# Optimization experiments

Measured on AMD Instinct MI355X. Metric: run time of the kernel, lower is better.

The kernel has to match this reference:

```python
import jax, jax.numpy as jnp
import numpy as np

B, L, D, H = 2, 2048, 1024, 16


def setup_inputs() -> dict:
    key = jax.random.key(0)
    ks = jax.random.split(key, 6)
    return {
        "x": jax.random.normal(ks[0], (B, L, D), dtype=jnp.float32),
        "w_qkv": jax.random.normal(ks[1], (3 * D, D), dtype=jnp.float32) * (D ** -0.5),
        "b_qkv": jax.random.normal(ks[2], (3 * D,), dtype=jnp.float32) * 0.02,
        "w_out": jax.random.normal(ks[3], (D, D), dtype=jnp.float32) * (D ** -0.5),
        "b_out": jax.random.normal(ks[4], (D,), dtype=jnp.float32) * 0.02,
        "lam": jnp.float32(0.5),
        "heads": H,
    }


def reference(x, w_qkv, b_qkv, w_out, b_out, lam, heads):
    b, l, d = x.shape
    dh = d // heads
    scale = d ** -0.5  # NOTE: module scales by d_model**-0.5, not head_dim**-0.5

    qkv = x @ w_qkv.T + b_qkv                      # [B, L, 3D]
    qkv = qkv.reshape(b, l, 3, heads, dh)
    qkv = jnp.transpose(qkv, (2, 0, 3, 1, 4))      # [3, B, H, L, dh]
    q, k, v = qkv[0], qkv[1], qkv[2]

    k_prev = jnp.roll(k, shift=1, axis=2)          # roll along sequence dim

    s_cur = jnp.einsum("bhqd,bhkd->bhqk", q, k) * scale
    s_prev = jnp.einsum("bhqd,bhkd->bhqk", q, k_prev) * scale

    a1 = jax.nn.softmax(s_cur, axis=-1)
    a2 = jax.nn.softmax(s_prev, axis=-1)
    diff = lam * (a1 - a2)                         # dropout = identity (eval)

    o = jnp.einsum("bhqk,bhkd->bhqd", diff, v)     # [B, H, L, dh]
    o = jnp.transpose(o, (0, 2, 1, 3)).reshape(b, l, d)
    return o @ w_out.T + b_out
```

## Files before the change

### kernel.cpp

```cpp
#include <hip/hip_runtime.h>
#include <hip/hip_bf16.h>
#include <stdint.h>


typedef __attribute__((ext_vector_type(8))) short s16x8;
typedef __attribute__((ext_vector_type(4))) short s16x4;
typedef __attribute__((ext_vector_type(4))) float f32x4;
typedef __attribute__((ext_vector_type(4))) unsigned int u32x4;

__device__ __forceinline__ float bf2f(unsigned short u) {
    union { unsigned int i; float f; } x; x.i = ((unsigned int)u) << 16; return x.f;
}
__device__ __forceinline__ unsigned short f2bf(float f) {
    union { float f; unsigned int i; } x; x.f = f;
    unsigned int r = x.i + 0x7FFFu + ((x.i >> 16) & 1u);
    return (unsigned short)(r >> 16);
}

__device__ __forceinline__ void gload16(const void* g, void* l) {
    auto gp = reinterpret_cast<const __attribute__((address_space(1))) unsigned int*>(
        reinterpret_cast<uintptr_t>(g));
    auto lp = reinterpret_cast<__attribute__((address_space(3))) unsigned int*>(
        reinterpret_cast<uintptr_t>(l));
    __builtin_amdgcn_global_load_lds(gp, lp, 16, 0, 0);
}

__global__ __launch_bounds__(256) void cvt_all(
    const float* __restrict__ x, const float* __restrict__ wq,
    const float* __restrict__ wo,
    unsigned short* __restrict__ xb, unsigned short* __restrict__ wqb,
    unsigned short* __restrict__ wob)
{
    int i4 = blockIdx.x * 256 + threadIdx.x;
    const float* src; unsigned short* dst; int off;
    if (i4 < 1048576)            { src = x;  dst = xb;  off = i4; }
    else if (i4 < 1048576 + 786432) { src = wq; dst = wqb; off = i4 - 1048576; }
    else                         { src = wo; dst = wob; off = i4 - 1835008; }
    float4 v = ((const float4*)src)[off];
    ushort4 u;
    u.x = f2bf(v.x); u.y = f2bf(v.y); u.z = f2bf(v.z); u.w = f2bf(v.w);
    ((ushort4*)dst)[off] = u;
}

__global__ __launch_bounds__(256) void vd_transpose(
    const unsigned short* __restrict__ qkvb, unsigned short* __restrict__ vdt)
{
    __shared__ unsigned short T[64][72];
    const int tid = threadIdx.x;
    const int j0 = blockIdx.x * 64;
    const int bh = blockIdx.y, b = bh >> 4, h = bh & 15;
    const unsigned short* vb = qkvb + (size_t)b * 2048 * 3072 + 2048 + h * 64;

    int r = tid >> 2, cq = tid & 3;
    int rp = (r & 35) | ((r & 12) << 1) | ((r & 16) >> 2);
    int j = j0 + r, jn = (j + 1) & 2047;
    const unsigned short* p0 = vb + (size_t)j  * 3072 + cq * 16;
    const unsigned short* p1 = vb + (size_t)jn * 3072 + cq * 16;
    s16x8 a0 = *(const s16x8*)p0, a1 = *(const s16x8*)(p0 + 8);
    s16x8 b0 = *(const s16x8*)p1, b1 = *(const s16x8*)(p1 + 8);
#pragma unroll
    for (int u = 0; u < 8; ++u)
        T[cq * 16 + u][rp] = f2bf(bf2f((unsigned short)a0[u]) - bf2f((unsigned short)b0[u]));
#pragma unroll
    for (int u = 0; u < 8; ++u)
        T[cq * 16 + 8 + u][rp] = f2bf(bf2f((unsigned short)a1[u]) - bf2f((unsigned short)b1[u]));
    __syncthreads();

    int row = tid >> 2, sc = tid & 3;
    s16x8 o0 = *(const s16x8*)&T[row][sc * 16];
    s16x8 o1 = *(const s16x8*)&T[row][sc * 16 + 8];
    unsigned short* dst = vdt + ((size_t)bh * 64 + row) * 2048 + j0 + sc * 16;
    *(s16x8*)dst = o0;
    *(s16x8*)(dst + 8) = o1;
}

template <int OUT_BF16, int BN>
__global__ __launch_bounds__(256) void gemm_nt_mfma(
    const unsigned short* __restrict__ A,
    const unsigned short* __restrict__ Bm,
    const float* __restrict__ bias,
    void* __restrict__ C,
    int M, int N, int K, int nscale, float smul)
{
    constexpr int NT = BN / 32;
    __shared__ unsigned short As[2][128][32];
    __shared__ unsigned short Bs[2][BN][32];

    const int tid = threadIdx.x;
    const int wave = tid >> 6, lane = tid & 63;
    const int quad = lane >> 4, ln = lane & 15;
    const int wm = (wave >> 1) * 64, wn = (wave & 1) * (NT * 16);
    const int m0 = blockIdx.y * 128, n0 = blockIdx.x * BN;
    const int rA = wave * 16 + (lane >> 2);
    const int gsl = lane & 3;

    f32x4 acc[4][NT];
#pragma unroll
    for (int mt = 0; mt < 4; ++mt)
#pragma unroll
        for (int nt = 0; nt < NT; ++nt) acc[mt][nt] = f32x4{0.f, 0.f, 0.f, 0.f};

    auto stage = [&](int p, int k0) {
#pragma unroll
        for (int q = 0; q < 2; ++q) {
            int row = q * 64 + rA;
            int kg = gsl ^ ((row >> 1) & 3);
            gload16(A + (size_t)(m0 + row) * K + k0 + kg * 8,
                    &As[p][q * 64 + wave * 16][0]);
            if (q * 64 < BN)
                gload16(Bm + (size_t)(n0 + row) * K + k0 + kg * 8,
                        &Bs[p][q * 64 + wave * 16][0]);
        }
    };

    stage(0, 0);
    __syncthreads();
    int p = 0;
    for (int k0 = 0; k0 < K; k0 += 32) {
        if (k0 + 32 < K) stage(p ^ 1, k0 + 32);
        s16x8 af[4], bfr[NT];
#pragma unroll
        for (int mt = 0; mt < 4; ++mt) {
            int rr = wm + mt * 16 + ln;
            af[mt] = *(const s16x8*)&As[p][rr][((quad ^ ((rr >> 1) & 3)) & 3) * 8];
        }
#pragma unroll
        for (int nt = 0; nt < NT; ++nt) {
            int rr = wn + nt * 16 + ln;
            bfr[nt] = *(const s16x8*)&Bs[p][rr][((quad ^ ((rr >> 1) & 3)) & 3) * 8];
        }
#pragma unroll
        for (int mt = 0; mt < 4; ++mt)
#pragma unroll
            for (int nt = 0; nt < NT; ++nt)
                acc[mt][nt] = __builtin_amdgcn_mfma_f32_16x16x32_bf16(
                    af[mt], bfr[nt], acc[mt][nt], 0, 0, 0);
        __syncthreads();
        p ^= 1;
    }

    float bb[NT];
#pragma unroll
    for (int nt = 0; nt < NT; ++nt) bb[nt] = bias[n0 + wn + nt * 16 + ln];
#pragma unroll
    for (int mt = 0; mt < 4; ++mt)
#pragma unroll
        for (int nt = 0; nt < NT; ++nt) {
            int col = n0 + wn + nt * 16 + ln;
            float sc = (col < nscale) ? smul : 1.f;
#pragma unroll
            for (int rg = 0; rg < 4; ++rg) {
                int row = m0 + wm + mt * 16 + quad * 4 + rg;
                float v = (acc[mt][nt][rg] + bb[nt]) * sc;
                if (OUT_BF16)
                    ((unsigned short*)C)[(size_t)row * N + col] = f2bf(v);
                else
                    ((float*)C)[(size_t)row * N + col] = v;
            }
        }
}

__global__ __launch_bounds__(512) void diff_attn_v7(
    const unsigned short* __restrict__ qkv,
    const unsigned short* __restrict__ vdt,
    const float* __restrict__ lam_p,
    unsigned short* __restrict__ o_ws)
{
    constexpr int L = 2048, TD = 3072;

    __shared__ unsigned short Ks[2][64][64];
    __shared__ unsigned short Vs[2][64][64];
    __shared__ f32x4 Red[4][2][4][64];
    __shared__ float Lred[4][2][64];

    const int tid = threadIdx.x;
    const int wave = tid >> 6, lane = tid & 63;
    const int qw = wave & 3, jw = wave >> 2;
    const int quad = lane >> 4, ln = lane & 15;
    const int bh = blockIdx.y, b = bh >> 4, h = bh & 15;
    const int q0 = blockIdx.x * 128;
    const size_t seqbase = (size_t)b * L;
    const unsigned short* base = qkv + seqbase * TD + h * 64;
    const unsigned short* kb = base + 1024;
    const unsigned short* vbase = vdt + (size_t)bh * 64 * 2048;

    const int lsl = lane >> 3;
    const int cgl = (lane & 7) ^ lsl;

    s16x8 qf[2][2];
#pragma unroll
    for (int s = 0; s < 2; ++s) {
        const unsigned short* qrow =
            base + (size_t)(q0 + qw * 32 + s * 16 + ln) * TD;
        qf[s][0] = *(const s16x8*)(qrow + quad * 8);
        qf[s][1] = *(const s16x8*)(qrow + 32 + quad * 8);
    }

    auto stage = [&](int p, int j0) {
        const unsigned short* k0p = kb + (size_t)(j0 + wave * 8 + lsl) * TD + cgl * 8;
        gload16(k0p, &Ks[p][wave * 8][0]);
        const unsigned short* v0p = vbase + (size_t)(wave * 8 + lsl) * 2048 + j0 + cgl * 8;
        gload16(v0p, &Vs[p][wave * 8][0]);
    };

    f32x4 Ot[2][4];
    f32x4 lacc[2];
#pragma unroll
    for (int s = 0; s < 2; ++s) {
        lacc[s] = f32x4{0.f, 0.f, 0.f, 0.f};
#pragma unroll
        for (int mt = 0; mt < 4; ++mt) Ot[s][mt] = f32x4{0.f, 0.f, 0.f, 0.f};
    }

    const s16x8 ones8 = {(short)0x3F80, (short)0x3F80, (short)0x3F80, (short)0x3F80,
                         (short)0x3F80, (short)0x3F80, (short)0x3F80, (short)0x3F80};
    const int kx0 = (quad ^ (ln & 7)) << 3;
    const int kx1 = ((quad + 4) ^ (ln & 7)) << 3;
    const int vx  = (((jw * 4 + quad) ^ (ln & 7))) << 3;

    stage(0, 0);
    __syncthreads();
    int p = 0;
    for (int kt = 0; kt < 32; ++kt) {
        if (kt + 1 < 32) stage(p ^ 1, (kt + 1) * 64);

        f32x4 ST[2][2];
#pragma unroll
        for (int t = 0; t < 2; ++t) {
            const int t2 = jw * 2 + t;
            s16x8 k0 = *(const s16x8*)&Ks[p][t2 * 16 + ln][kx0];
            s16x8 k1 = *(const s16x8*)&Ks[p][t2 * 16 + ln][kx1];
#pragma unroll
            for (int s = 0; s < 2; ++s) {
                f32x4 z = f32x4{0.f, 0.f, 0.f, 0.f};
                z = __builtin_amdgcn_mfma_f32_16x16x32_bf16(k0, qf[s][0], z, 0, 0, 0);
                z = __builtin_amdgcn_mfma_f32_16x16x32_bf16(k1, qf[s][1], z, 0, 0, 0);
                ST[s][t] = z;
            }
        }

        s16x8 pf8[2];
#pragma unroll
        for (int s = 0; s < 2; ++s) {
            unsigned int w[4];
#pragma unroll
            for (int t = 0; t < 2; ++t) {
                unsigned int b0 = __builtin_bit_cast(unsigned int,
                    __builtin_amdgcn_exp2f(ST[s][t][0]));
                unsigned int b1 = __builtin_bit_cast(unsigned int,
                    __builtin_amdgcn_exp2f(ST[s][t][1]));
                unsigned int b2 = __builtin_bit_cast(unsigned int,
                    __builtin_amdgcn_exp2f(ST[s][t][2]));
                unsigned int b3 = __builtin_bit_cast(unsigned int,
                    __builtin_amdgcn_exp2f(ST[s][t][3]));
                w[t * 2]     = (b0 >> 16) | (b1 & 0xFFFF0000u);
                w[t * 2 + 1] = (b2 >> 16) | (b3 & 0xFFFF0000u);
            }
            pf8[s] = __builtin_bit_cast(s16x8, (u32x4){w[0], w[1], w[2], w[3]});
        }

#pragma unroll
        for (int s = 0; s < 2; ++s)
            lacc[s] = __builtin_amdgcn_mfma_f32_16x16x32_bf16(
                ones8, pf8[s], lacc[s], 0, 0, 0);

#pragma unroll
        for (int mt = 0; mt < 4; ++mt) {
            s16x8 vf = *(const s16x8*)&Vs[p][mt * 16 + ln][vx];
#pragma unroll
            for (int s = 0; s < 2; ++s)
                Ot[s][mt] = __builtin_amdgcn_mfma_f32_16x16x32_bf16(
                    vf, pf8[s], Ot[s][mt], 0, 0, 0);
        }
        __syncthreads();
        p ^= 1;
    }

    if (jw == 1) {
#pragma unroll
        for (int s = 0; s < 2; ++s) {
            Lred[qw][s][lane] = lacc[s][0];
#pragma unroll
            for (int mt = 0; mt < 4; ++mt) Red[qw][s][mt][lane] = Ot[s][mt];
        }
    }
    __syncthreads();
    if (jw == 0) {
        const float lam = lam_p[0];
#pragma unroll
        for (int s = 0; s < 2; ++s) {
            float lsum = lacc[s][0] + Lred[qw][s][lane];
            float inv = lam / lsum;
            int row = q0 + qw * 32 + s * 16 + ln;
            unsigned short* orow = o_ws + (seqbase + row) * 1024 + h * 64 + quad * 4;
#pragma unroll
            for (int mt = 0; mt < 4; ++mt) {
                f32x4 r = Red[qw][s][mt][lane];
                ushort4 u;
                u.x = f2bf((Ot[s][mt][0] + r[0]) * inv);
                u.y = f2bf((Ot[s][mt][1] + r[1]) * inv);
                u.z = f2bf((Ot[s][mt][2] + r[2]) * inv);
                u.w = f2bf((Ot[s][mt][3] + r[3]) * inv);
                *(ushort4*)(orow + mt * 16) = u;
            }
        }
    }
}

extern "C" void kernel_launch(void* const* d_in, const int* in_sizes, int n_in,
                              void* d_out, int out_size, void* d_ws, size_t ws_size,
                              hipStream_t stream) {
    const float* x     = (const float*)d_in[0];
    const float* w_qkv = (const float*)d_in[1];
    const float* b_qkv = (const float*)d_in[2];
    const float* w_out = (const float*)d_in[3];
    const float* b_out = (const float*)d_in[4];
    const float* lam   = (const float*)d_in[5];
    float* out = (float*)d_out;

    unsigned short* xb   = (unsigned short*)d_ws;
    unsigned short* wqb  = xb   + (size_t)4096 * 1024;
    unsigned short* wob  = wqb  + (size_t)3072 * 1024;
    unsigned short* qkvb = wob  + (size_t)1024 * 1024;
    unsigned short* ob   = qkvb + (size_t)4096 * 3072;
    unsigned short* vdt  = ob   + (size_t)4096 * 1024;

    cvt_all<<<8192, 256, 0, stream>>>(x, w_qkv, w_out, xb, wqb, wob);

    gemm_nt_mfma<1, 128><<<dim3(24, 32), 256, 0, stream>>>(
        xb, wqb, b_qkv, qkvb, 4096, 3072, 1024, 1024, 0.045084222f);

    vd_transpose<<<dim3(32, 32), 256, 0, stream>>>(qkvb, vdt);

    diff_attn_v7<<<dim3(16, 32), 512, 0, stream>>>(qkvb, vdt, lam, ob);

    gemm_nt_mfma<0, 64><<<dim3(16, 32), 256, 0, stream>>>(
        ob, wob, b_out, out, 4096, 1024, 1024, 0, 1.f);
}
```

Before: 186.3 us.

## Triple-buffer K/V tiles in attention kernel with vmcnt-gated barriers

```diff
diff --git a/kernel.cpp b/kernel.cpp
--- a/kernel.cpp
+++ b/kernel.cpp
@@ -160,7 +160,7 @@
         }
 }
 
-__global__ __launch_bounds__(512) void diff_attn_v7(
+__global__ __launch_bounds__(512) void diff_attn_v8(
     const unsigned short* __restrict__ qkv,
     const unsigned short* __restrict__ vdt,
     const float* __restrict__ lam_p,
@@ -168,10 +168,11 @@
 {
     constexpr int L = 2048, TD = 3072;
 
-    __shared__ unsigned short Ks[2][64][64];
-    __shared__ unsigned short Vs[2][64][64];
-    __shared__ f32x4 Red[4][2][4][64];
-    __shared__ float Lred[4][2][64];
+    __shared__ __align__(16) unsigned char smem[49152];
+    auto Ks = reinterpret_cast<unsigned short(*)[64][64]>(smem);
+    auto Vs = reinterpret_cast<unsigned short(*)[64][64]>(smem + 24576);
+    auto Red = reinterpret_cast<f32x4(*)[2][4][64]>(smem);
+    auto Lred = reinterpret_cast<float(*)[2][64]>(smem + 32768);
 
     const int tid = threadIdx.x;
     const int wave = tid >> 6, lane = tid & 63;
@@ -187,6 +188,9 @@
     const int lsl = lane >> 3;
     const int cgl = (lane & 7) ^ lsl;
 
+    const float lam = lam_p[0];
+    asm volatile("" :: "v"(lam));
+
     s16x8 qf[2][2];
 #pragma unroll
     for (int s = 0; s < 2; ++s) {
@@ -219,17 +223,20 @@
     const int vx  = (((jw * 4 + quad) ^ (ln & 7))) << 3;
 
     stage(0, 0);
-    __syncthreads();
-    int p = 0;
+    stage(1, 64);
+    asm volatile("s_waitcnt vmcnt(2)" ::: "memory");
+    __builtin_amdgcn_s_barrier();
+
+    int cur = 0, nx2 = 2;
     for (int kt = 0; kt < 32; ++kt) {
-        if (kt + 1 < 32) stage(p ^ 1, (kt + 1) * 64);
+        stage(nx2, ((kt + 2) & 31) * 64);
 
         f32x4 ST[2][2];
 #pragma unroll
         for (int t = 0; t < 2; ++t) {
             const int t2 = jw * 2 + t;
-            s16x8 k0 = *(const s16x8*)&Ks[p][t2 * 16 + ln][kx0];
-            s16x8 k1 = *(const s16x8*)&Ks[p][t2 * 16 + ln][kx1];
+            s16x8 k0 = *(const s16x8*)&Ks[cur][t2 * 16 + ln][kx0];
+            s16x8 k1 = *(const s16x8*)&Ks[cur][t2 * 16 + ln][kx1];
 #pragma unroll
             for (int s = 0; s < 2; ++s) {
                 f32x4 z = f32x4{0.f, 0.f, 0.f, 0.f};
@@ -266,15 +273,22 @@
 
 #pragma unroll
         for (int mt = 0; mt < 4; ++mt) {
-            s16x8 vf = *(const s16x8*)&Vs[p][mt * 16 + ln][vx];
+            s16x8 vf = *(const s16x8*)&Vs[cur][mt * 16 + ln][vx];
 #pragma unroll
             for (int s = 0; s < 2; ++s)
                 Ot[s][mt] = __builtin_amdgcn_mfma_f32_16x16x32_bf16(
                     vf, pf8[s], Ot[s][mt], 0, 0, 0);
         }
-        __syncthreads();
-        p ^= 1;
-    }
+
+        asm volatile("s_waitcnt vmcnt(2)" ::: "memory");
+        __builtin_amdgcn_s_barrier();
+        asm volatile("" ::: "memory");
+
+        cur = (cur == 2) ? 0 : cur + 1;
+        nx2 = (nx2 == 2) ? 0 : nx2 + 1;
+    }
+
+    __syncthreads();
 
     if (jw == 1) {
 #pragma unroll
@@ -286,7 +300,6 @@
     }
     __syncthreads();
     if (jw == 0) {
-        const float lam = lam_p[0];
 #pragma unroll
         for (int s = 0; s < 2; ++s) {
             float lsum = lacc[s][0] + Lred[qw][s][lane];
@@ -332,7 +345,7 @@
 
     vd_transpose<<<dim3(32, 32), 256, 0, stream>>>(qkvb, vdt);
 
-    diff_attn_v7<<<dim3(16, 32), 512, 0, stream>>>(qkvb, vdt, lam, ob);
+    diff_attn_v8<<<dim3(16, 32), 512, 0, stream>>>(qkvb, vdt, lam, ob);
 
     gemm_nt_mfma<0, 64><<<dim3(16, 32), 256, 0, stream>>>(
         ob, wob, b_out, out, 4096, 1024, 1024, 0, 1.f);
```

New measurement: 181.8 us. 2.4% less time.
